# Kernel optimization log

Hardware: AMD Instinct MI355X
Metric: run time of the kernel (lower is better)

## Reference

```python
import jax, jax.numpy as jnp
import numpy as np

N_HEADS = 16
D_HEAD = 64
THETA = 10000.0


def _rope_tables(S, dh, dtype):
    inv_freq = 1.0 / (THETA ** (jnp.arange(0, dh, 2, dtype=jnp.float32) / dh))  # [dh/2]
    ang = jnp.arange(S, dtype=jnp.float32)[:, None] * inv_freq[None, :]  # [S, dh/2]
    return jnp.cos(ang).astype(dtype), jnp.sin(ang).astype(dtype)


def _apply_rope(t, cos, sin):
    # t: [B,S,H,dh]; interleaved complex pairs (even=real, odd=imag)
    B, S, H, dh = t.shape
    tr = t.reshape(B, S, H, dh // 2, 2)
    a, b = tr[..., 0], tr[..., 1]
    c = cos[None, :, None, :]
    s = sin[None, :, None, :]
    ra = a * c - b * s
    rb = a * s + b * c
    return jnp.stack([ra, rb], axis=-1).reshape(B, S, H, dh)


def setup_inputs() -> dict:
    key = jax.random.key(0)
    ks = jax.random.split(key, 5)
    B, S, D = 2, 2048, 1024
    x = jax.random.normal(ks[0], (B, S, D), dtype=jnp.float32)
    scale = 1.0 / np.sqrt(D)
    wq = jax.random.normal(ks[1], (D, D), dtype=jnp.float32) * scale
    wk = jax.random.normal(ks[2], (D, D), dtype=jnp.float32) * scale
    wv = jax.random.normal(ks[3], (D, D), dtype=jnp.float32) * scale
    wo = jax.random.normal(ks[4], (D, D), dtype=jnp.float32) * scale
    return {"x": x, "wq": wq, "wk": wk, "wv": wv, "wo": wo}


def reference(x, wq, wk, wv, wo):
    B, S, D = x.shape
    H, dh = N_HEADS, D_HEAD
    q = (x @ wq).reshape(B, S, H, dh)
    k = (x @ wk).reshape(B, S, H, dh)
    v = (x @ wv).reshape(B, S, H, dh)
    cos, sin = _rope_tables(S, dh, x.dtype)
    q = _apply_rope(q, cos, sin)
    k = _apply_rope(k, cos, sin)
    # [B,H,S,S] scores
    scale = 1.0 / np.sqrt(dh).astype(np.float32)
    attn = jnp.einsum('bqhd,bkhd->bhqk', q, k) * scale
    causal = jnp.tril(jnp.ones((S, S), dtype=bool))[None, None]
    attn = jnp.where(causal, attn, -jnp.inf)
    probs = jax.nn.softmax(attn, axis=-1)
    head_out = jnp.einsum('bhqk,bkhd->bqhd', probs, v).reshape(B, S, D)
    return head_out @ wo
```

## Files before the change

### kernel.cpp

```cpp
#include <hip/hip_runtime.h>
#include <hip/hip_bf16.h>

#define S_LEN   2048
#define BATCH   2
#define NH      16
#define DH      64
#define DMODEL  1024
#define MTOT    (BATCH * S_LEN)

typedef __attribute__((ext_vector_type(4))) float f32x4;
typedef __attribute__((ext_vector_type(8))) short s16x8;
typedef __attribute__((ext_vector_type(4))) short s16x4;

#define MFMA_BF16(a, b, c) __builtin_amdgcn_mfma_f32_16x16x32_bf16((a), (b), (c), 0, 0, 0)

static __device__ __forceinline__ short f2bf(float f) {
    union { float f; unsigned u; } v; v.f = f;
    unsigned r = v.u + 0x7fffu + ((v.u >> 16) & 1u);
    return (short)(r >> 16);
}

static __device__ __forceinline__ unsigned cvtpk_bf16(float lo, float hi) {
    unsigned r;
    asm volatile("v_cvt_pk_bf16_f32 %0, %1, %2" : "=v"(r) : "v"(lo), "v"(hi));
    return r;
}

static __device__ __forceinline__ void gload_lds16(const void* g, void* l) {
    __builtin_amdgcn_global_load_lds(
        (const __attribute__((address_space(1))) void*)g,
        (__attribute__((address_space(3))) void*)l, 16, 0, 0);
}

#define VM_WAIT(N) asm volatile("s_waitcnt vmcnt(" #N ")" ::: "memory")
static __device__ __forceinline__ void barrier_raw() {
    __builtin_amdgcn_sched_barrier(0);
    __builtin_amdgcn_s_barrier();
    __builtin_amdgcn_sched_barrier(0);
}

__global__ __launch_bounds__(256) void prep_wt(const float* __restrict__ wq,
                                               const float* __restrict__ wk,
                                               const float* __restrict__ wv,
                                               const float* __restrict__ wo,
                                               short* __restrict__ wtb) {
    const float* W = (blockIdx.z == 0) ? wq : (blockIdx.z == 1) ? wk
                   : (blockIdx.z == 2) ? wv : wo;
    short* out = wtb + (size_t)blockIdx.z * DMODEL * DMODEL;

    __shared__ short T[64][72];
    const int t  = threadIdx.x;
    const int k0 = blockIdx.y * 64, n0 = blockIdx.x * 64;

    #pragma unroll
    for (int p = 0; p < 4; ++p) {
        const int kk = p * 16 + (t >> 4);
        const int nn = (t & 15) * 4;
        f32x4 v = *(const f32x4*)(W + (size_t)(k0 + kk) * DMODEL + n0 + nn);
        #pragma unroll
        for (int j = 0; j < 4; ++j) T[nn + j][kk] = f2bf(v[j]);
    }
    __syncthreads();
    #pragma unroll
    for (int p = 0; p < 4; ++p) {
        const int nn = p * 16 + (t >> 4);
        const int kk = (t & 15) * 4;
        *(s16x4*)(out + (size_t)(n0 + nn) * DMODEL + k0 + kk) = *(const s16x4*)&T[nn][kk];
    }
}

__global__ __launch_bounds__(256) void prep_x(const float* __restrict__ x,
                                              short* __restrict__ xb) {
    const size_t i = (size_t)(blockIdx.x * 256 + threadIdx.x) * 8;
    f32x4 a = *(const f32x4*)(x + i);
    f32x4 b = *(const f32x4*)(x + i + 4);
    s16x8 o;
    #pragma unroll
    for (int j = 0; j < 4; ++j) { o[j] = f2bf(a[j]); o[4 + j] = f2bf(b[j]); }
    *(s16x8*)(xb + i) = o;
}

__global__ __launch_bounds__(256) void prep_rope(float* __restrict__ cosT,
                                                 float* __restrict__ sinT) {
    const int idx = blockIdx.x * 256 + threadIdx.x;
    const int s = idx >> 5, i = idx & 31;
    const float inv = exp2f(-(float)i * (13.287712379549449f / 32.0f));
    const float ang = (float)s * inv;
    cosT[idx] = cosf(ang);
    sinT[idx] = sinf(ang);
}

__device__ __forceinline__ void gemm_tile(const short* __restrict__ A,
                                          const short* __restrict__ Bt,
                                          f32x4 acc[4][4]) {
    __shared__ __align__(16) short As[3][4096];
    __shared__ __align__(16) short Bs[3][4096];
    const int tid  = threadIdx.x;
    const int lane = tid & 63;
    const int wv   = tid >> 6;
    const int wm   = (wv >> 1) * 64;
    const int wn   = (wv & 1) * 64;
    const int g = lane >> 4, c16 = lane & 15;
    const int m0 = blockIdx.y * 128;
    const int n0 = blockIdx.x * 128;

    const int srow = tid >> 2;
    const int schk = (tid & 3) ^ (srow & 3);
    const short* ga0 = A  + (size_t)(m0 + srow)      * DMODEL + schk * 8;
    const short* ga1 = A  + (size_t)(m0 + 64 + srow) * DMODEL + schk * 8;
    const short* gb0 = Bt + (size_t)(n0 + srow)      * DMODEL + schk * 8;
    const short* gb1 = Bt + (size_t)(n0 + 64 + srow) * DMODEL + schk * 8;
    const int lw = wv * 512;

    #define STAGE_G(buf, ko) do { \
        gload_lds16(ga0 + (ko), &As[buf][lw]); \
        gload_lds16(ga1 + (ko), &As[buf][2048 + lw]); \
        gload_lds16(gb0 + (ko), &Bs[buf][lw]); \
        gload_lds16(gb1 + (ko), &Bs[buf][2048 + lw]); \
    } while (0)

    STAGE_G(0, 0);
    STAGE_G(1, 32);

    const int rchk = (g ^ (c16 & 3)) << 3;
    for (int ks = 0; ks < 32; ++ks) {
        if (ks < 31) { VM_WAIT(4); } else { VM_WAIT(0); }
        barrier_raw();
        if (ks + 2 < 32) STAGE_G((ks + 2) % 3, (ks + 2) * 32);
        const int cur = ks % 3;
        s16x8 af[4], bfr[4];
        #pragma unroll
        for (int i = 0; i < 4; ++i)
            af[i] = *(const s16x8*)&As[cur][(wm + i * 16 + c16) * 32 + rchk];
        #pragma unroll
        for (int j = 0; j < 4; ++j)
            bfr[j] = *(const s16x8*)&Bs[cur][(wn + j * 16 + c16) * 32 + rchk];
        __builtin_amdgcn_s_setprio(1);
        #pragma unroll
        for (int i = 0; i < 4; ++i)
            #pragma unroll
            for (int j = 0; j < 4; ++j)
                acc[i][j] = MFMA_BF16(af[i], bfr[j], acc[i][j]);
        __builtin_amdgcn_s_setprio(0);
    }
    #undef STAGE_G
}

__global__ __launch_bounds__(256) void gemm_qkv(const short* __restrict__ xb,
                                                const short* __restrict__ wtb,
                                                short* __restrict__ Qo,
                                                short* __restrict__ Ko,
                                                short* __restrict__ Vt,
                                                const float* __restrict__ cosT,
                                                const float* __restrict__ sinT) {
    const int z = blockIdx.z;
    const short* Bt = wtb + (size_t)z * DMODEL * DMODEL;

    f32x4 acc[4][4] = {};
    gemm_tile(xb, Bt, acc);

    const int tid  = threadIdx.x;
    const int lane = tid & 63;
    const int wv   = tid >> 6;
    const int wm   = (wv >> 1) * 64, wn = (wv & 1) * 64;
    const int g = lane >> 4, c16 = lane & 15;
    const int m0 = blockIdx.y * 128, n0 = blockIdx.x * 128;

    if (z < 2) {
        short* out = (z == 0) ? Qo : Ko;
        const float post = (z == 0) ? 0.18033688011112042f : 1.0f;
        #pragma unroll
        for (int j = 0; j < 4; ++j) {
            const int n = n0 + wn + j * 16 + c16;
            const int h = n >> 6, d = n & 63;
            #pragma unroll
            for (int i = 0; i < 4; ++i) {
                #pragma unroll
                for (int r = 0; r < 4; ++r) {
                    const int m = m0 + wm + i * 16 + g * 4 + r;
                    const int s = m & (S_LEN - 1);
                    const int b = m >> 11;
                    float v = acc[i][j][r];
                    float vo = __shfl_xor(v, 1, 64);
                    float cs = cosT[s * 32 + (d >> 1)];
                    float sn = sinT[s * 32 + (d >> 1)];
                    float res = (d & 1) ? (vo * sn + v * cs) : (v * cs - vo * sn);
                    res *= post;
                    out[(((size_t)b * NH + h) * S_LEN + s) * DH + d] = f2bf(res);
                }
            }
        }
    } else {
        #pragma unroll
        for (int j = 0; j < 4; ++j) {
            const int n = n0 + wn + j * 16 + c16;
            const int h = n >> 6, d = n & 63;
            #pragma unroll
            for (int i = 0; i < 4; ++i) {
                const int mb = m0 + wm + i * 16 + g * 4;
                const int b  = mb >> 11;
                const int sr = mb & (S_LEN - 1);
                s16x4 pk;
                #pragma unroll
                for (int r = 0; r < 4; ++r) pk[r] = f2bf(acc[i][j][r]);
                *(s16x4*)(Vt + (((size_t)b * NH + h) * DH + d) * S_LEN + sr) = pk;
            }
        }
    }
}

__global__ __launch_bounds__(256) void attn(const short* __restrict__ Q,
                                            const short* __restrict__ K,
                                            const short* __restrict__ Vt,
                                            short* __restrict__ O) {
    const int tid  = threadIdx.x;
    const int lane = tid & 63;
    const int w    = tid >> 6;
    const int g = lane >> 4, c16 = lane & 15;
    const int bid  = blockIdx.x + 16 * blockIdx.y;
    const int cxcd = bid & 7, jj = bid >> 3;
    const int bh   = (jj & 3) * 8 + cxcd;
    const int bx   = jj >> 2;
    const size_t base = (size_t)bh * S_LEN * DH;
    const short* Kb = K + base;
    const short* Vb = Vt + (size_t)bh * DH * S_LEN;
    const int b = bh >> 4, h = bh & 15;

    __shared__ __align__(16) short KL[3][4096];
    __shared__ __align__(16) short VL[3][4096];
    __shared__ __align__(16) short P2[4][16][72];

    const int kr = tid >> 3;
    const int kc = (tid & 7) ^ (kr & 7);
    const short* kg0 = Kb + (size_t)kr * DH + (kc << 3);
    const short* kg1 = Kb + (size_t)(32 + kr) * DH + (kc << 3);
    const short* vg0 = Vb + (size_t)kr * S_LEN + (kc << 3);
    const short* vg1 = Vb + (size_t)(32 + kr) * S_LEN + (kc << 3);
    const int lw = w * 512;
    const int kx = c16 & 7;

    #pragma unroll 1
    for (int half = 0; half < 2; ++half) {
        const int ci = half ? bx : 31 - bx;
        const int ntiles = ci + 1;
        const int wq0 = ci * 64 + w * 16;

        gload_lds16(kg0, &KL[0][lw]);
        gload_lds16(kg1, &KL[0][2048 + lw]);
        gload_lds16(vg0, &VL[0][lw]);
        gload_lds16(vg1, &VL[0][2048 + lw]);
        s16x8 bq0 = *(const s16x8*)(Q + base + (size_t)(wq0 + c16) * DH + g * 8);
        s16x8 bq1 = *(const s16x8*)(Q + base + (size_t)(wq0 + c16) * DH + 32 + g * 8);
        if (ntiles > 1) {
            gload_lds16(kg0 + (size_t)64 * DH, &KL[1][lw]);
            gload_lds16(kg1 + (size_t)64 * DH, &KL[1][2048 + lw]);
            gload_lds16(vg0 + 64, &VL[1][lw]);
            gload_lds16(vg1 + 64, &VL[1][2048 + lw]);
        }

        f32x4 o[4] = {};
        float lsum = 0.f;

        for (int tt = 0; tt < ntiles; ++tt) {
            if (tt + 1 < ntiles) { VM_WAIT(4); } else { VM_WAIT(0); }
            barrier_raw();
            if (tt + 2 < ntiles) {
                const int nb = (tt + 2) % 3;
                const size_t ko = (size_t)(tt + 2) * 64;
                gload_lds16(kg0 + ko * DH, &KL[nb][lw]);
                gload_lds16(kg1 + ko * DH, &KL[nb][2048 + lw]);
                gload_lds16(vg0 + ko,      &VL[nb][lw]);
                gload_lds16(vg1 + ko,      &VL[nb][2048 + lw]);
            }
            const int cur = tt % 3;

            f32x4 s[4];
            __builtin_amdgcn_s_setprio(1);
            #pragma unroll
            for (int cg = 0; cg < 4; ++cg) {
                const int krow = (cg * 16 + c16) * 64;
                s16x8 kf0 = *(const s16x8*)&KL[cur][krow + ((g ^ kx) << 3)];
                s16x8 kf1 = *(const s16x8*)&KL[cur][krow + (((4 + g) ^ kx) << 3)];
                f32x4 zz = {};
                zz = MFMA_BF16(kf0, bq0, zz);
                s[cg] = MFMA_BF16(kf1, bq1, zz);
            }
            __builtin_amdgcn_s_setprio(0);

            s16x8 vf[4][2];
            #pragma unroll
            for (int nt = 0; nt < 4; ++nt) {
                const int vr = (nt * 16 + c16) * 64;
                vf[nt][0] = *(const s16x8*)&VL[cur][vr + ((g ^ kx) << 3)];
                vf[nt][1] = *(const s16x8*)&VL[cur][vr + (((4 + g) ^ kx) << 3)];
            }

            const bool diag = (tt == ci);
            const int qrel = w * 16 + c16;
            #pragma unroll
            for (int cg = 0; cg < 4; ++cg) {
                float e[4];
                #pragma unroll
                for (int r = 0; r < 4; ++r) {
                    e[r] = exp2f(s[cg][r]);
                    if (diag && (cg * 16 + g * 4 + r > qrel)) e[r] = 0.f;
                }
                lsum += (e[0] + e[1]) + (e[2] + e[3]);
                uint2 pk;
                pk.x = cvtpk_bf16(e[0], e[1]);
                pk.y = cvtpk_bf16(e[2], e[3]);
                *(uint2*)&P2[w][c16][cg * 16 + g * 4] = pk;
            }
            asm volatile("s_waitcnt lgkmcnt(0)" ::: "memory");
            __builtin_amdgcn_sched_barrier(0);
            s16x8 ap0 = *(const s16x8*)&P2[w][c16][g * 8];
            s16x8 ap1 = *(const s16x8*)&P2[w][c16][32 + g * 8];

            __builtin_amdgcn_s_setprio(1);
            #pragma unroll
            for (int nt = 0; nt < 4; ++nt) {
                o[nt] = MFMA_BF16(ap0, vf[nt][0], o[nt]);
                o[nt] = MFMA_BF16(ap1, vf[nt][1], o[nt]);
            }
            __builtin_amdgcn_s_setprio(0);
        }

        float lt = lsum;
        lt += __shfl_xor(lt, 16, 64);
        lt += __shfl_xor(lt, 32, 64);
        #pragma unroll
        for (int r = 0; r < 4; ++r) {
            const float linv = 1.0f / __shfl(lt, g * 4 + r, 64);
            #pragma unroll
            for (int nt = 0; nt < 4; ++nt) {
                O[((size_t)(b * S_LEN + wq0 + g * 4 + r)) * DMODEL
                  + h * DH + nt * 16 + c16] = f2bf(o[nt][r] * linv);
            }
        }
    }
}

__global__ __launch_bounds__(256) void gemm_o(const short* __restrict__ Ob,
                                              const short* __restrict__ WoT,
                                              float* __restrict__ C) {
    f32x4 acc[4][4] = {};
    gemm_tile(Ob, WoT, acc);

    const int tid  = threadIdx.x;
    const int lane = tid & 63;
    const int wv   = tid >> 6;
    const int wm   = (wv >> 1) * 64, wn = (wv & 1) * 64;
    const int g = lane >> 4, c16 = lane & 15;
    const int m0 = blockIdx.y * 128, n0 = blockIdx.x * 128;

    #pragma unroll
    for (int i = 0; i < 4; ++i)
        #pragma unroll
        for (int j = 0; j < 4; ++j) {
            const int n = n0 + wn + j * 16 + c16;
            #pragma unroll
            for (int r = 0; r < 4; ++r) {
                const int m = m0 + wm + i * 16 + g * 4 + r;
                C[(size_t)m * DMODEL + n] = acc[i][j][r];
            }
        }
}

extern "C" void kernel_launch(void* const* d_in, const int* in_sizes, int n_in,
                              void* d_out, int out_size, void* d_ws, size_t ws_size,
                              hipStream_t stream) {
    const float* x  = (const float*)d_in[0];
    const float* wq = (const float*)d_in[1];
    const float* wk = (const float*)d_in[2];
    const float* wv = (const float*)d_in[3];
    const float* wo = (const float*)d_in[4];
    float* out = (float*)d_out;

    char* ws = (char*)d_ws;
    short* wtb  = (short*)ws;
    short* xb   = (short*)(ws + (8ull  << 20));
    float* cosT = (float*)(ws + (16ull << 20));
    float* sinT = (float*)(ws + (16ull << 20) + (256ull << 10));
    short* Qb   = (short*)(ws + (17ull << 20));
    short* Kb   = (short*)(ws + (25ull << 20));
    short* Vtb  = (short*)(ws + (33ull << 20));
    short* Ob   = (short*)(ws + (41ull << 20));

    prep_wt  <<<dim3(16, 16, 4), 256, 0, stream>>>(wq, wk, wv, wo, wtb);
    prep_x   <<<dim3(2048),      256, 0, stream>>>(x, xb);
    prep_rope<<<dim3(256),       256, 0, stream>>>(cosT, sinT);

    gemm_qkv<<<dim3(8, 32, 3), 256, 0, stream>>>(xb, wtb, Qb, Kb, Vtb, cosT, sinT);
    attn    <<<dim3(16, 32),  256, 0, stream>>>(Qb, Kb, Vtb, Ob);
    gemm_o  <<<dim3(8, 32),   256, 0, stream>>>(Ob, wtb + 3ull * DMODEL * DMODEL, out);
}
```

Measured before the change: 135.0 us.

## Remap GEMM tile order for XCD locality, change LDS swizzle, drop setprio

Both GEMM kernels now compute their tile coordinates from a remapped block id. Consecutive tiles are grouped so that blocks dispatched round-robin across the 8 XCDs land near each other and share A/B panels in L2. The QKV GEMM is flattened into one 24x32 grid over the concatenated weight matrices, with z derived from the column tile. The LDS XOR swizzle changes from row-based to a (row>>1)-based pattern, aimed at fewer bank conflicts for 16-byte reads, and the s_setprio hints around the MFMA loop are removed. The remap assumes a specific hardware dispatch order, and the new swizzle has to stay consistent between the writer and the reader.

```diff
diff --git a/kernel.cpp b/kernel.cpp
--- a/kernel.cpp
+++ b/kernel.cpp
@@ -92,6 +92,7 @@
 
 __device__ __forceinline__ void gemm_tile(const short* __restrict__ A,
                                           const short* __restrict__ Bt,
+                                          int m0, int n0,
                                           f32x4 acc[4][4]) {
     __shared__ __align__(16) short As[3][4096];
     __shared__ __align__(16) short Bs[3][4096];
@@ -101,11 +102,9 @@
     const int wm   = (wv >> 1) * 64;
     const int wn   = (wv & 1) * 64;
     const int g = lane >> 4, c16 = lane & 15;
-    const int m0 = blockIdx.y * 128;
-    const int n0 = blockIdx.x * 128;
 
     const int srow = tid >> 2;
-    const int schk = (tid & 3) ^ (srow & 3);
+    const int schk = (tid & 3) ^ ((tid >> 3) & 3);
     const short* ga0 = A  + (size_t)(m0 + srow)      * DMODEL + schk * 8;
     const short* ga1 = A  + (size_t)(m0 + 64 + srow) * DMODEL + schk * 8;
     const short* gb0 = Bt + (size_t)(n0 + srow)      * DMODEL + schk * 8;
@@ -122,7 +121,8 @@
     STAGE_G(0, 0);
     STAGE_G(1, 32);
 
-    const int rchk = (g ^ (c16 & 3)) << 3;
+    const int rsw  = (c16 >> 1) & 3;
+    const int rlo  = (g ^ rsw) << 3;
     for (int ks = 0; ks < 32; ++ks) {
         if (ks < 31) { VM_WAIT(4); } else { VM_WAIT(0); }
         barrier_raw();
@@ -131,17 +131,15 @@
         s16x8 af[4], bfr[4];
         #pragma unroll
         for (int i = 0; i < 4; ++i)
-            af[i] = *(const s16x8*)&As[cur][(wm + i * 16 + c16) * 32 + rchk];
+            af[i] = *(const s16x8*)&As[cur][(wm + i * 16 + c16) * 32 + rlo];
         #pragma unroll
         for (int j = 0; j < 4; ++j)
-            bfr[j] = *(const s16x8*)&Bs[cur][(wn + j * 16 + c16) * 32 + rchk];
-        __builtin_amdgcn_s_setprio(1);
+            bfr[j] = *(const s16x8*)&Bs[cur][(wn + j * 16 + c16) * 32 + rlo];
         #pragma unroll
         for (int i = 0; i < 4; ++i)
             #pragma unroll
             for (int j = 0; j < 4; ++j)
                 acc[i][j] = MFMA_BF16(af[i], bfr[j], acc[i][j]);
-        __builtin_amdgcn_s_setprio(0);
     }
     #undef STAGE_G
 }
@@ -153,18 +151,20 @@
                                                 short* __restrict__ Vt,
                                                 const float* __restrict__ cosT,
                                                 const float* __restrict__ sinT) {
-    const int z = blockIdx.z;
-    const short* Bt = wtb + (size_t)z * DMODEL * DMODEL;
+    const int dd = blockIdx.x + 24 * blockIdx.y;
+    const int ti = (dd & 7) * 96 + (dd >> 3);
+    const int tx = ti % 24, ty = ti / 24;
+    const int m0 = ty * 128, n0 = tx * 128;
+    const int z  = tx >> 3;
 
     f32x4 acc[4][4] = {};
-    gemm_tile(xb, Bt, acc);
+    gemm_tile(xb, wtb, m0, n0, acc);
 
     const int tid  = threadIdx.x;
     const int lane = tid & 63;
     const int wv   = tid >> 6;
     const int wm   = (wv >> 1) * 64, wn = (wv & 1) * 64;
     const int g = lane >> 4, c16 = lane & 15;
-    const int m0 = blockIdx.y * 128, n0 = blockIdx.x * 128;
 
     if (z < 2) {
         short* out = (z == 0) ? Qo : Ko;
@@ -172,7 +172,8 @@
         #pragma unroll
         for (int j = 0; j < 4; ++j) {
             const int n = n0 + wn + j * 16 + c16;
-            const int h = n >> 6, d = n & 63;
+            const int nz = n & 1023;
+            const int h = nz >> 6, d = nz & 63;
             #pragma unroll
             for (int i = 0; i < 4; ++i) {
                 #pragma unroll
@@ -194,7 +195,8 @@
         #pragma unroll
         for (int j = 0; j < 4; ++j) {
             const int n = n0 + wn + j * 16 + c16;
-            const int h = n >> 6, d = n & 63;
+            const int nz = n & 1023;
+            const int h = nz >> 6, d = nz & 63;
             #pragma unroll
             for (int i = 0; i < 4; ++i) {
                 const int mb = m0 + wm + i * 16 + g * 4;
@@ -343,15 +345,19 @@
 __global__ __launch_bounds__(256) void gemm_o(const short* __restrict__ Ob,
                                               const short* __restrict__ WoT,
                                               float* __restrict__ C) {
+    const int dd = blockIdx.x + 8 * blockIdx.y;
+    const int ti = (dd & 7) * 32 + (dd >> 3);
+    const int tx = ti & 7, ty = ti >> 3;
+    const int m0 = ty * 128, n0 = tx * 128;
+
     f32x4 acc[4][4] = {};
-    gemm_tile(Ob, WoT, acc);
+    gemm_tile(Ob, WoT, m0, n0, acc);
 
     const int tid  = threadIdx.x;
     const int lane = tid & 63;
     const int wv   = tid >> 6;
     const int wm   = (wv >> 1) * 64, wn = (wv & 1) * 64;
     const int g = lane >> 4, c16 = lane & 15;
-    const int m0 = blockIdx.y * 128, n0 = blockIdx.x * 128;
 
     #pragma unroll
     for (int i = 0; i < 4; ++i)
@@ -390,7 +396,7 @@
     prep_x   <<<dim3(2048),      256, 0, stream>>>(x, xb);
     prep_rope<<<dim3(256),       256, 0, stream>>>(cosT, sinT);
 
-    gemm_qkv<<<dim3(8, 32, 3), 256, 0, stream>>>(xb, wtb, Qb, Kb, Vtb, cosT, sinT);
-    attn    <<<dim3(16, 32),  256, 0, stream>>>(Qb, Kb, Vtb, Ob);
-    gemm_o  <<<dim3(8, 32),   256, 0, stream>>>(Ob, wtb + 3ull * DMODEL * DMODEL, out);
-}
+    gemm_qkv<<<dim3(24, 32), 256, 0, stream>>>(xb, wtb, Qb, Kb, Vtb, cosT, sinT);
+    attn    <<<dim3(16, 32), 256, 0, stream>>>(Qb, Kb, Vtb, Ob);
+    gemm_o  <<<dim3(8, 32),  256, 0, stream>>>(Ob, wtb + 3ull * DMODEL * DMODEL, out);
+}
```

Result: no change. 137.5 us (+1.8%).
